# Optimization experiments

Hardware: AMD Instinct MI355X
Metric: run time of the kernel (lower is better)

Reference implementation:

```python
import jax, jax.numpy as jnp
import numpy as np

N, E = 50000, 800000
IN_DIM, HID, L, H = 128, 128, 3, 4
C = HID // H  # per-head channels
NEG_SLOPE = 0.2


def layer_norm(x, g, b, eps=1e-5):
    mu = jnp.mean(x, axis=-1, keepdims=True)
    var = jnp.var(x, axis=-1, keepdims=True)
    return (x - mu) * jax.lax.rsqrt(var + eps) * g + b


def gatv2_conv(x, edge_index, Wl, bl, Wr, br, att, conv_b):
    # x: [N, HID]; edge_index: [2, E]; Wl/Wr: [HID, HID]; att: [H, C]
    src, dst = edge_index[0], edge_index[1]
    xl = (x @ Wl + bl).reshape(N, H, C)  # source transform
    xr = (x @ Wr + br).reshape(N, H, C)  # target transform
    e = jax.nn.leaky_relu(xl[src] + xr[dst], NEG_SLOPE)      # [E, H, C]
    alpha = jnp.einsum('ehc,hc->eh', e, att)                  # [E, H]
    # segment softmax over incoming edges of each dst node
    amax = jax.ops.segment_max(alpha, dst, num_segments=N)    # [N, H]
    ex = jnp.exp(alpha - amax[dst])
    denom = jax.ops.segment_sum(ex, dst, num_segments=N)[dst] + 1e-16
    w = ex / denom                                            # [E, H]
    out = jax.ops.segment_sum(xl[src] * w[:, :, None], dst, num_segments=N)
    return out.reshape(N, HID) + conv_b


def setup_inputs() -> dict:
    key = jax.random.key(0)
    ks = jax.random.split(key, 24)
    s = 0.05
    inp = {
        'x': jax.random.normal(ks[0], (N, IN_DIM), jnp.float32),
        'edge_index': jax.random.randint(ks[1], (2, E), 0, N, jnp.int64),
        'Win': jax.random.normal(ks[2], (IN_DIM, HID)) * s,
        'b_in': jnp.zeros((HID,)),
        'ln_g': jnp.ones((L, HID)),
        'ln_b': jnp.zeros((L, HID)),
        'Wl': jax.random.normal(ks[3], (L, HID, HID)) * s,
        'bl': jnp.zeros((L, HID)),
        'Wr': jax.random.normal(ks[4], (L, HID, HID)) * s,
        'br': jnp.zeros((L, HID)),
        'att': jax.random.normal(ks[5], (L, H, C)) * s,
        'conv_b': jnp.zeros((L, HID)),
        'fn_g': jnp.ones((HID,)),
        'fn_b': jnp.zeros((HID,)),
        'pW1': jax.random.normal(ks[6], (HID, HID // 2)) * s,
        'pb1': jnp.zeros((HID // 2,)),
        'pW2': jax.random.normal(ks[7], (HID // 2, 1)) * s,
        'pb2': jnp.zeros((1,)),
        'vW1': jax.random.normal(ks[8], (HID, HID // 2)) * s,
        'vb1': jnp.zeros((HID // 2,)),
        'vW2': jax.random.normal(ks[9], (HID // 2, HID)) * s,
        'vb2': jnp.zeros((HID,)),
    }
    return inp


def reference(x, edge_index, Win, b_in, ln_g, ln_b, Wl, bl, Wr, br, att, conv_b,
              fn_g, fn_b, pW1, pb1, pW2, pb2, vW1, vb1, vW2, vb2):
    h = x @ Win + b_in  # input_proj
    # GNNResidualBlock (assumed pre-norm residual): h = h + gelu(conv(LN(h)))
    for i in range(L):
        z = layer_norm(h, ln_g[i], ln_b[i])
        z = gatv2_conv(z, edge_index, Wl[i], bl[i], Wr[i], br[i], att[i], conv_b[i])
        h = h + jax.nn.gelu(z)
    h = layer_norm(h, fn_g, fn_b)
    prob_logits = jax.nn.gelu(h @ pW1 + pb1) @ pW2 + pb2   # [N, 1]
    volume_emb = jax.nn.gelu(h @ vW1 + vb1) @ vW2 + vb2     # [N, HID]
    return (volume_emb, prob_logits)
```

## Files before the change

kernel.cpp:

```cpp
#include <hip/hip_runtime.h>
#include <math.h>

constexpr int NN  = 50000;
constexpr int EE  = 800000;
constexpr int NPAD = 50176;

typedef short bf16x8 __attribute__((ext_vector_type(8)));
typedef float f32x4  __attribute__((ext_vector_type(4)));

__device__ __forceinline__ unsigned f2bfu(float f) {
    union { float f; unsigned u; } x; x.f = f;
    unsigned r = x.u + 0x7fffu + ((x.u >> 16) & 1u);
    return r >> 16;
}
__device__ __forceinline__ short f2bf(float f) { return (short)f2bfu(f); }
__device__ __forceinline__ unsigned pack2(float lo, float hi) {
    return f2bfu(lo) | (f2bfu(hi) << 16);
}
__device__ __forceinline__ float bfbits_lo(unsigned w) { return __uint_as_float(w << 16); }
__device__ __forceinline__ float bfbits_hi(unsigned w) { return __uint_as_float(w & 0xffff0000u); }

__device__ __forceinline__ float gelu_tanh(float x) {
    float u = 0.7978845608028654f * (x + 0.044715f * x * x * x);
    float t = 1.0f - 2.0f / (__expf(2.0f * u) + 1.0f);
    return 0.5f * x * (1.0f + t);
}

__device__ __forceinline__ float dpp_add16(float x) {
    int t;
    t = __builtin_amdgcn_update_dpp(0, __float_as_int(x), 0xB1,  0xf, 0xf, true);
    x += __int_as_float(t);
    t = __builtin_amdgcn_update_dpp(0, __float_as_int(x), 0x4E,  0xf, 0xf, true);
    x += __int_as_float(t);
    t = __builtin_amdgcn_update_dpp(0, __float_as_int(x), 0x141, 0xf, 0xf, true);
    x += __int_as_float(t);
    t = __builtin_amdgcn_update_dpp(0, __float_as_int(x), 0x140, 0xf, 0xf, true);
    x += __int_as_float(t);
    return x;
}

struct WtArgs {
    const float* src[10];
    short*       dst[10];
    int K[10];
    int N[10];
};

template<int BN, int NB, int DO_LN, int ACT, int OUTBF0, int OUTBF1>
__device__ __forceinline__ void ln_gemm_body(
    int row0, const float* __restrict__ A,
    const float* __restrict__ lg, const float* __restrict__ lb,
    const short* __restrict__ B0t, const float* __restrict__ bias0, void* __restrict__ C0,
    const short* __restrict__ B1t, const float* __restrict__ bias1, void* __restrict__ C1,
    int nrows, short* As, short* Bs)
{
    constexpr int K = 128, KP = 136;
    constexpr int NF = BN / 16;
    constexpr int CH = K / 8;
    const int tid = threadIdx.x;

    {
        int r = tid >> 2, q = tid & 3;
        int grow = row0 + r;
        bool ok = grow < nrows;
        float4 v[8];
        const float* src = A + (size_t)grow * K + q * 32;
#pragma unroll
        for (int i = 0; i < 8; ++i)
            v[i] = ok ? *reinterpret_cast<const float4*>(src + i * 4)
                      : make_float4(0.f, 0.f, 0.f, 0.f);
        if (DO_LN) {
            float s = 0.f, s2 = 0.f;
#pragma unroll
            for (int i = 0; i < 8; ++i) {
                s  += v[i].x + v[i].y + v[i].z + v[i].w;
                s2 += v[i].x * v[i].x + v[i].y * v[i].y + v[i].z * v[i].z + v[i].w * v[i].w;
            }
            s += __shfl_xor(s, 1); s2 += __shfl_xor(s2, 1);
            s += __shfl_xor(s, 2); s2 += __shfl_xor(s2, 2);
            float mean = s * (1.f / 128.f);
            float var  = s2 * (1.f / 128.f) - mean * mean;
            float rstd = rsqrtf(var + 1e-5f);
#pragma unroll
            for (int i = 0; i < 8; ++i) {
                float4 gg = *reinterpret_cast<const float4*>(lg + q * 32 + i * 4);
                float4 bb = *reinterpret_cast<const float4*>(lb + q * 32 + i * 4);
                v[i].x = (v[i].x - mean) * rstd * gg.x + bb.x;
                v[i].y = (v[i].y - mean) * rstd * gg.y + bb.y;
                v[i].z = (v[i].z - mean) * rstd * gg.z + bb.z;
                v[i].w = (v[i].w - mean) * rstd * gg.w + bb.w;
            }
        }
        short* dst = &As[r * KP + q * 32];
#pragma unroll
        for (int i = 0; i < 4; ++i) {
            uint4 w = make_uint4(pack2(v[2*i].x,   v[2*i].y),
                                 pack2(v[2*i].z,   v[2*i].w),
                                 pack2(v[2*i+1].x, v[2*i+1].y),
                                 pack2(v[2*i+1].z, v[2*i+1].w));
            *reinterpret_cast<uint4*>(dst + i * 8) = w;
        }
    }

    auto stageB = [&](const short* __restrict__ Bt) {
#pragma unroll
        for (int it = 0; it < BN * CH / 256; ++it) {
            int idx = tid + it * 256;
            int nn = idx / CH, j = idx % CH;
            *reinterpret_cast<uint4*>(&Bs[nn * KP + j * 8]) =
                *reinterpret_cast<const uint4*>(&Bt[nn * K + j * 8]);
        }
    };
    stageB(B0t);
    __syncthreads();

    const int wave = tid >> 6;
    const int lane = tid & 63;
    const int kg   = lane >> 4;
    const int lr   = lane & 15;

    bf16x8 afrag[4];
#pragma unroll
    for (int kk = 0; kk < 4; ++kk)
        afrag[kk] = *reinterpret_cast<const bf16x8*>(
            &As[(wave * 16 + lr) * KP + kk * 32 + kg * 8]);

    auto do_gemm = [&](const float* __restrict__ bias, void* __restrict__ Cv, bool outbf) {
        f32x4 acc[NF];
#pragma unroll
        for (int nf = 0; nf < NF; ++nf) acc[nf] = (f32x4){0.f, 0.f, 0.f, 0.f};
#pragma unroll
        for (int nf = 0; nf < NF; ++nf) {
#pragma unroll
            for (int kk = 0; kk < 4; ++kk) {
                bf16x8 bfrag = *reinterpret_cast<const bf16x8*>(
                    &Bs[(nf * 16 + lr) * KP + kk * 32 + kg * 8]);
                acc[nf] = __builtin_amdgcn_mfma_f32_16x16x32_bf16(
                    afrag[kk], bfrag, acc[nf], 0, 0, 0);
            }
        }
#pragma unroll
        for (int nf = 0; nf < NF; ++nf) {
            int col = nf * 16 + lr;
            float bi = bias[col];
#pragma unroll
            for (int j = 0; j < 4; ++j) {
                int row = row0 + wave * 16 + kg * 4 + j;
                if (row < nrows) {
                    float v = acc[nf][j] + bi;
                    if (ACT == 1) v = gelu_tanh(v);
                    if (outbf) ((short*)Cv)[(size_t)row * BN + col] = f2bf(v);
                    else       ((float*)Cv)[(size_t)row * BN + col] = v;
                }
            }
        }
    };

    do_gemm(bias0, C0, OUTBF0 != 0);
    if (NB == 2) {
        __syncthreads();
        stageB(B1t);
        __syncthreads();
        do_gemm(bias1, C1, OUTBF1 != 0);
    }
}

__global__ __launch_bounds__(256) void hybrid1(
    const int* __restrict__ ei, int* __restrict__ counts, int* __restrict__ pos, WtArgs a)
{
    if (blockIdx.x < 1024) {
        for (int e = blockIdx.x * 256 + threadIdx.x; e < EE; e += 1024 * 256)
            pos[e] = atomicAdd(&counts[ei[EE + e]], 1);
    } else {
        int bb = blockIdx.x - 1024;
        int m = bb >> 4, slice = bb & 15;
        const float* s = a.src[m];
        short* d = a.dst[m];
        int K = a.K[m], N = a.N[m], total = K * N;
        for (int i = slice * 256 + threadIdx.x; i < total; i += 16 * 256) {
            int k = i / N, n = i - k * N;
            d[n * K + k] = f2bf(s[i]);
        }
    }
}

__device__ void scan256(const int* __restrict__ counts, int* __restrict__ roff) {
    __shared__ int wsum[4];
    __shared__ int tilesum;
    int tid = threadIdx.x, wid = tid >> 6, lane = tid & 63;
    int carry = 0;
    for (int base = 0; base < NPAD; base += 1024) {
        int idx = base + tid * 4;
        int4 c = *reinterpret_cast<const int4*>(&counts[idx]);
        int s0 = c.x, s1 = s0 + c.y, s2 = s1 + c.z, s3 = s2 + c.w;
        int x = s3;
#pragma unroll
        for (int off = 1; off < 64; off <<= 1) {
            int t = __shfl_up(x, off);
            if (lane >= off) x += t;
        }
        if (lane == 63) wsum[wid] = x;
        __syncthreads();
        if (tid == 0) {
            int a0 = wsum[0], a1 = wsum[1], a2 = wsum[2], a3 = wsum[3];
            wsum[0] = 0; wsum[1] = a0; wsum[2] = a0 + a1; wsum[3] = a0 + a1 + a2;
            tilesum = a0 + a1 + a2 + a3;
        }
        __syncthreads();
        int start = carry + wsum[wid] + (x - s3);
        int4 o = make_int4(start, start + s0, start + s1, start + s2);
        *reinterpret_cast<int4*>(&roff[idx]) = o;
        carry += tilesum;
        __syncthreads();
    }
}

__global__ __launch_bounds__(256) void hybrid2(
    const int* __restrict__ counts, int* __restrict__ roff,
    const float* __restrict__ x, const short* __restrict__ Win_t,
    const float* __restrict__ b_in, float* __restrict__ h, int nrows)
{
    __shared__ short As[64 * 136];
    __shared__ short Bs[128 * 136];
    if (blockIdx.x == 0) {
        scan256(counts, roff);
    } else {
        ln_gemm_body<128, 1, 0, 0, 0, 0>((blockIdx.x - 1) * 64, x, nullptr, nullptr,
            Win_t, b_in, h, nullptr, nullptr, nullptr, nrows, As, Bs);
    }
}

__global__ __launch_bounds__(256) void hybrid3(
    const int* __restrict__ ei, const int* __restrict__ roff,
    const int* __restrict__ pos, int* __restrict__ ssrc,
    const float* __restrict__ h, const float* __restrict__ lg, const float* __restrict__ lb,
    const short* __restrict__ Wl_t, const float* __restrict__ bl, short* __restrict__ XL,
    const short* __restrict__ Wr_t, const float* __restrict__ br, short* __restrict__ XR,
    int nrows)
{
    __shared__ short As[64 * 136];
    __shared__ short Bs[128 * 136];
    if (blockIdx.x < 512) {
        for (int e = blockIdx.x * 256 + threadIdx.x; e < EE; e += 512 * 256)
            ssrc[roff[ei[EE + e]] + pos[e]] = ei[e] << 8;
    } else {
        ln_gemm_body<128, 2, 1, 0, 1, 1>((blockIdx.x - 512) * 64, h, lg, lb,
            Wl_t, bl, XL, Wr_t, br, XR, nrows, As, Bs);
    }
}

__global__ __launch_bounds__(256) void fused_layer(
    const float* __restrict__ h, const float* __restrict__ lg, const float* __restrict__ lb,
    const short* __restrict__ Wl_t, const float* __restrict__ bl, short* __restrict__ XL,
    const short* __restrict__ Wr_t, const float* __restrict__ br, short* __restrict__ XR,
    int nrows)
{
    __shared__ short As[64 * 136];
    __shared__ short Bs[128 * 136];
    ln_gemm_body<128, 2, 1, 0, 1, 1>(blockIdx.x * 64, h, lg, lb,
        Wl_t, bl, XL, Wr_t, br, XR, nrows, As, Bs);
}

__global__ __launch_bounds__(256) void gat_node_kernel(
    const short* __restrict__ XL, const short* __restrict__ XR,
    const int* __restrict__ roff, const int* __restrict__ ssrc,
    const float* __restrict__ att, const float* __restrict__ conv_b,
    float* __restrict__ h)
{
    int n = blockIdx.x * 4 + (threadIdx.x >> 6);
    if (n >= NN) return;
    int lane = threadIdx.x & 63;
    int j0 = lane * 2;
    unsigned wr = *reinterpret_cast<const unsigned*>(&XR[(size_t)n * 128 + j0]);
    float xr0 = bfbits_lo(wr), xr1 = bfbits_hi(wr);
    float2 at = *reinterpret_cast<const float2*>(&att[j0]);

    float dA = 0.f, a0A = 0.f, a1A = 0.f;
    float dB = 0.f, a0B = 0.f, a1B = 0.f;

    const char* XLb = (const char*)XL;
    const unsigned lbyte = (unsigned)lane * 4u;

    auto proc = [&](unsigned w, float& d, float& a0, float& a1) {
        float x0 = bfbits_lo(w), x1 = bfbits_hi(w);
        float e0 = x0 + xr0; e0 = fmaxf(e0, 0.2f * e0);
        float e1 = x1 + xr1; e1 = fmaxf(e1, 0.2f * e1);
        float part = fmaf(e1, at.y, e0 * at.x);
        part = dpp_add16(part);
        float pe = __expf(part);
        d += pe;
        a0 = fmaf(pe, x0, a0);
        a1 = fmaf(pe, x1, a1);
    };

    int beg = roff[n], end = roff[n + 1], p = beg;
    for (; p + 3 < end; p += 4) {
        unsigned o0 = (unsigned)ssrc[p]     + lbyte;
        unsigned o1 = (unsigned)ssrc[p + 1] + lbyte;
        unsigned o2 = (unsigned)ssrc[p + 2] + lbyte;
        unsigned o3 = (unsigned)ssrc[p + 3] + lbyte;
        unsigned w0 = *reinterpret_cast<const unsigned*>(XLb + o0);
        unsigned w1 = *reinterpret_cast<const unsigned*>(XLb + o1);
        unsigned w2 = *reinterpret_cast<const unsigned*>(XLb + o2);
        unsigned w3 = *reinterpret_cast<const unsigned*>(XLb + o3);
        proc(w0, dA, a0A, a1A);
        proc(w1, dB, a0B, a1B);
        proc(w2, dA, a0A, a1A);
        proc(w3, dB, a0B, a1B);
    }
    for (; p < end; ++p) {
        unsigned w0 = *reinterpret_cast<const unsigned*>(
            XLb + ((unsigned)ssrc[p] + lbyte));
        proc(w0, dA, a0A, a1A);
    }
    float d    = dA + dB;
    float acc0 = a0A + a0B;
    float acc1 = a1A + a1B;

    float inv = 1.f / (d + 1e-16f);
    float2 cb = *reinterpret_cast<const float2*>(&conv_b[j0]);
    float o0 = gelu_tanh(fmaf(acc0, inv, cb.x));
    float o1 = gelu_tanh(fmaf(acc1, inv, cb.y));
    float2 hv = *reinterpret_cast<const float2*>(&h[(size_t)n * 128 + j0]);
    hv.x += o0; hv.y += o1;
    *reinterpret_cast<float2*>(&h[(size_t)n * 128 + j0]) = hv;
}

__global__ __launch_bounds__(256) void final_head_full(
    const float* __restrict__ A,
    const float* __restrict__ lg, const float* __restrict__ lb,
    const short* __restrict__ pW1t, const float* __restrict__ pb1,
    const float* __restrict__ pW2, const float* __restrict__ pb2,
    const short* __restrict__ vW1t, const float* __restrict__ vb1,
    const short* __restrict__ vW2t, const float* __restrict__ vb2,
    float* __restrict__ vol, float* __restrict__ prob, int nrows)
{
    constexpr int K = 128, KP = 136, KP2 = 72;
    constexpr int CH = K / 8;
    __shared__ short As[64 * 136];
    __shared__ short Bs[128 * 136];

    const int tid  = threadIdx.x;
    const int row0 = blockIdx.x * 64;

    {
        int r = tid >> 2, q = tid & 3;
        int grow = row0 + r;
        bool ok = grow < nrows;
        float4 v[8];
        const float* src = A + (size_t)grow * K + q * 32;
#pragma unroll
        for (int i = 0; i < 8; ++i)
            v[i] = ok ? *reinterpret_cast<const float4*>(src + i * 4)
                      : make_float4(0.f, 0.f, 0.f, 0.f);
        float s = 0.f, s2 = 0.f;
#pragma unroll
        for (int i = 0; i < 8; ++i) {
            s  += v[i].x + v[i].y + v[i].z + v[i].w;
            s2 += v[i].x * v[i].x + v[i].y * v[i].y + v[i].z * v[i].z + v[i].w * v[i].w;
        }
        s += __shfl_xor(s, 1); s2 += __shfl_xor(s2, 1);
        s += __shfl_xor(s, 2); s2 += __shfl_xor(s2, 2);
        float mean = s * (1.f / 128.f);
        float var  = s2 * (1.f / 128.f) - mean * mean;
        float rstd = rsqrtf(var + 1e-5f);
        short* dst = &As[r * KP + q * 32];
#pragma unroll
        for (int i = 0; i < 8; ++i) {
            float4 gg = *reinterpret_cast<const float4*>(lg + q * 32 + i * 4);
            float4 bb = *reinterpret_cast<const float4*>(lb + q * 32 + i * 4);
            v[i].x = (v[i].x - mean) * rstd * gg.x + bb.x;
            v[i].y = (v[i].y - mean) * rstd * gg.y + bb.y;
            v[i].z = (v[i].z - mean) * rstd * gg.z + bb.z;
            v[i].w = (v[i].w - mean) * rstd * gg.w + bb.w;
        }
#pragma unroll
        for (int i = 0; i < 4; ++i) {
            uint4 w = make_uint4(pack2(v[2*i].x,   v[2*i].y),
                                 pack2(v[2*i].z,   v[2*i].w),
                                 pack2(v[2*i+1].x, v[2*i+1].y),
                                 pack2(v[2*i+1].z, v[2*i+1].w));
            *reinterpret_cast<uint4*>(dst + i * 8) = w;
        }
    }
#pragma unroll
    for (int it = 0; it < 8; ++it) {
        int idx = tid + it * 256;
        int nn = idx / CH, j = idx % CH;
        const short* srcw = (nn < 64) ? &pW1t[nn * K + j * 8]
                                      : &vW1t[(nn - 64) * K + j * 8];
        *reinterpret_cast<uint4*>(&Bs[nn * KP + j * 8]) =
            *reinterpret_cast<const uint4*>(srcw);
    }
    __syncthreads();

    const int wave = tid >> 6;
    const int lane = tid & 63;
    const int kg   = lane >> 4;
    const int lr   = lane & 15;

    bf16x8 afrag[4];
#pragma unroll
    for (int kk = 0; kk < 4; ++kk)
        afrag[kk] = *reinterpret_cast<const bf16x8*>(
            &As[(wave * 16 + lr) * KP + kk * 32 + kg * 8]);

    f32x4 acc_v[4];
#pragma unroll
    for (int nf = 0; nf < 4; ++nf) acc_v[nf] = (f32x4){0.f, 0.f, 0.f, 0.f};
#pragma unroll
    for (int nf = 0; nf < 4; ++nf)
#pragma unroll
        for (int kk = 0; kk < 4; ++kk) {
            bf16x8 bfrag = *reinterpret_cast<const bf16x8*>(
                &Bs[(64 + nf * 16 + lr) * KP + kk * 32 + kg * 8]);
            acc_v[nf] = __builtin_amdgcn_mfma_f32_16x16x32_bf16(
                afrag[kk], bfrag, acc_v[nf], 0, 0, 0);
        }

    {
        f32x4 acc[4];
#pragma unroll
        for (int nf = 0; nf < 4; ++nf) acc[nf] = (f32x4){0.f, 0.f, 0.f, 0.f};
#pragma unroll
        for (int nf = 0; nf < 4; ++nf)
#pragma unroll
            for (int kk = 0; kk < 4; ++kk) {
                bf16x8 bfrag = *reinterpret_cast<const bf16x8*>(
                    &Bs[(nf * 16 + lr) * KP + kk * 32 + kg * 8]);
                acc[nf] = __builtin_amdgcn_mfma_f32_16x16x32_bf16(
                    afrag[kk], bfrag, acc[nf], 0, 0, 0);
            }
        float pr[4] = {0.f, 0.f, 0.f, 0.f};
#pragma unroll
        for (int nf = 0; nf < 4; ++nf) {
            int col = nf * 16 + lr;
            float bi = pb1[col];
            float w2 = pW2[col];
#pragma unroll
            for (int j = 0; j < 4; ++j)
                pr[j] = fmaf(gelu_tanh(acc[nf][j] + bi), w2, pr[j]);
        }
#pragma unroll
        for (int j = 0; j < 4; ++j) {
            float v = dpp_add16(pr[j]);
            int row = row0 + wave * 16 + kg * 4 + j;
            if (lr == 0 && row < nrows) prob[row] = v + pb2[0];
        }
    }

    __syncthreads();
    short* t2lds = As;
#pragma unroll
    for (int nf = 0; nf < 4; ++nf) {
        int col = nf * 16 + lr;
        float bi = vb1[col];
#pragma unroll
        for (int j = 0; j < 4; ++j) {
            int r = wave * 16 + kg * 4 + j;
            t2lds[r * KP2 + col] = f2bf(gelu_tanh(acc_v[nf][j] + bi));
        }
    }
#pragma unroll
    for (int it = 0; it < 4; ++it) {
        int idx = tid + it * 256;
        int nn = idx >> 3, j = idx & 7;
        *reinterpret_cast<uint4*>(&Bs[nn * KP2 + j * 8]) =
            *reinterpret_cast<const uint4*>(&vW2t[nn * 64 + j * 8]);
    }
    __syncthreads();

    bf16x8 a2[2];
#pragma unroll
    for (int kk = 0; kk < 2; ++kk)
        a2[kk] = *reinterpret_cast<const bf16x8*>(
            &t2lds[(wave * 16 + lr) * KP2 + kk * 32 + kg * 8]);
    f32x4 accv[8];
#pragma unroll
    for (int nf = 0; nf < 8; ++nf) accv[nf] = (f32x4){0.f, 0.f, 0.f, 0.f};
#pragma unroll
    for (int nf = 0; nf < 8; ++nf)
#pragma unroll
        for (int kk = 0; kk < 2; ++kk) {
            bf16x8 bfrag = *reinterpret_cast<const bf16x8*>(
                &Bs[(nf * 16 + lr) * KP2 + kk * 32 + kg * 8]);
            accv[nf] = __builtin_amdgcn_mfma_f32_16x16x32_bf16(
                a2[kk], bfrag, accv[nf], 0, 0, 0);
        }
#pragma unroll
    for (int nf = 0; nf < 8; ++nf) {
        int col = nf * 16 + lr;
        float bi = vb2[col];
#pragma unroll
        for (int j = 0; j < 4; ++j) {
            int row = row0 + wave * 16 + kg * 4 + j;
            if (row < nrows)
                vol[(size_t)row * 128 + col] = accv[nf][j] + bi;
        }
    }
}

extern "C" void kernel_launch(void* const* d_in, const int* in_sizes, int n_in,
                              void* d_out, int out_size, void* d_ws, size_t ws_size,
                              hipStream_t stream)
{
    const float* x      = (const float*)d_in[0];
    const int*   ei     = (const int*)  d_in[1];
    const float* Win    = (const float*)d_in[2];
    const float* b_in   = (const float*)d_in[3];
    const float* ln_g   = (const float*)d_in[4];
    const float* ln_b   = (const float*)d_in[5];
    const float* Wl     = (const float*)d_in[6];
    const float* bl     = (const float*)d_in[7];
    const float* Wr     = (const float*)d_in[8];
    const float* br     = (const float*)d_in[9];
    const float* att    = (const float*)d_in[10];
    const float* conv_b = (const float*)d_in[11];
    const float* fn_g   = (const float*)d_in[12];
    const float* fn_b   = (const float*)d_in[13];
    const float* pW1    = (const float*)d_in[14];
    const float* pb1    = (const float*)d_in[15];
    const float* pW2    = (const float*)d_in[16];
    const float* pb2    = (const float*)d_in[17];
    const float* vW1    = (const float*)d_in[18];
    const float* vb1    = (const float*)d_in[19];
    const float* vW2    = (const float*)d_in[20];
    const float* vb2    = (const float*)d_in[21];

    char* wp = (char*)d_ws;
    float* h   = (float*)wp;  wp += (size_t)NN * 128 * 4;
    short* XL  = (short*)wp;  wp += (size_t)NN * 128 * 2;
    short* XR  = (short*)wp;  wp += (size_t)NN * 128 * 2;
    int* counts = (int*)wp;   wp += (size_t)NPAD * 4;
    int* roff   = (int*)wp;   wp += (size_t)(NPAD + 16) * 4;
    int* pos    = (int*)wp;   wp += (size_t)EE * 4;
    int* ssrc   = (int*)wp;   wp += (size_t)EE * 4;
    short* Win_t = (short*)wp;
    short* Wl_t  = Win_t + 16384;
    short* Wr_t  = Wl_t + 3 * 16384;
    short* pW1_t = Wr_t + 3 * 16384;
    short* vW1_t = pW1_t + 8192;
    short* vW2_t = vW1_t + 8192;
    float* vol  = (float*)d_out;
    float* prob = (float*)d_out + (size_t)NN * 128;

    WtArgs wa;
    wa.src[0] = Win;  wa.dst[0] = Win_t; wa.K[0] = 128; wa.N[0] = 128;
    for (int i = 0; i < 3; ++i) {
        wa.src[1 + i] = Wl + (size_t)i * 16384; wa.dst[1 + i] = Wl_t + i * 16384;
        wa.K[1 + i] = 128; wa.N[1 + i] = 128;
        wa.src[4 + i] = Wr + (size_t)i * 16384; wa.dst[4 + i] = Wr_t + i * 16384;
        wa.K[4 + i] = 128; wa.N[4 + i] = 128;
    }
    wa.src[7] = pW1; wa.dst[7] = pW1_t; wa.K[7] = 128; wa.N[7] = 64;
    wa.src[8] = vW1; wa.dst[8] = vW1_t; wa.K[8] = 128; wa.N[8] = 64;
    wa.src[9] = vW2; wa.dst[9] = vW2_t; wa.K[9] = 64;  wa.N[9] = 128;

    const int gemm_grid = (NN + 63) / 64;
    const int row_grid  = (NN + 3) / 4;

    hipMemsetAsync(counts, 0, (size_t)NPAD * sizeof(int), stream);
    hybrid1<<<1024 + 160, 256, 0, stream>>>(ei, counts, pos, wa);
    hybrid2<<<1 + gemm_grid, 256, 0, stream>>>(counts, roff, x, Win_t, b_in, h, NN);
    hybrid3<<<512 + gemm_grid, 256, 0, stream>>>(ei, roff, pos, ssrc,
        h, ln_g, ln_b, Wl_t, bl, XL, Wr_t, br, XR, NN);
    gat_node_kernel<<<row_grid, 256, 0, stream>>>(
        XL, XR, roff, ssrc, att, conv_b, h);
    for (int i = 1; i < 3; ++i) {
        fused_layer<<<gemm_grid, 256, 0, stream>>>(
            h, ln_g + i * 128, ln_b + i * 128,
            Wl_t + i * 16384, bl + i * 128, XL,
            Wr_t + i * 16384, br + i * 128, XR, NN);
        gat_node_kernel<<<row_grid, 256, 0, stream>>>(
            XL, XR, roff, ssrc, att + i * 128, conv_b + i * 128, h);
    }
    final_head_full<<<gemm_grid, 256, 0, stream>>>(
        h, fn_g, fn_b, pW1_t, pb1, pW2, pb2, vW1_t, vb1, vW2_t, vb2, vol, prob, NN);
}
```

Measured before the change: 376.4 us.

## Replace stored edge positions with destination-partitioned atomic scatter; use exp2 in softmax

The CSR build no longer writes and reads back a per-edge position array. The scatter kernel now has each of 8 block groups handle one destination range and claim slots with a second atomic counter array, which removes 3.2MB of position traffic but makes every block scan its edge chunk 8 times. The attention softmax folds log2(e) into the attention vector and uses the native exp2 instruction instead of __expf. Edge order within each node becomes nondeterministic, which changes float summation order slightly.

```diff
diff --git a/kernel.cpp b/kernel.cpp
--- a/kernel.cpp
+++ b/kernel.cpp
@@ -4,6 +4,7 @@
 constexpr int NN  = 50000;
 constexpr int EE  = 800000;
 constexpr int NPAD = 50176;
+constexpr float LOG2E = 1.4426950408889634f;
 
 typedef short bf16x8 __attribute__((ext_vector_type(8)));
 typedef float f32x4  __attribute__((ext_vector_type(4)));
@@ -166,11 +167,11 @@
 }
 
 __global__ __launch_bounds__(256) void hybrid1(
-    const int* __restrict__ ei, int* __restrict__ counts, int* __restrict__ pos, WtArgs a)
+    const int* __restrict__ ei, int* __restrict__ counts, WtArgs a)
 {
     if (blockIdx.x < 1024) {
         for (int e = blockIdx.x * 256 + threadIdx.x; e < EE; e += 1024 * 256)
-            pos[e] = atomicAdd(&counts[ei[EE + e]], 1);
+            atomicAdd(&counts[ei[EE + e]], 1);
     } else {
         int bb = blockIdx.x - 1024;
         int m = bb >> 4, slice = bb & 15;
@@ -225,14 +226,14 @@
     if (blockIdx.x == 0) {
         scan256(counts, roff);
     } else {
-        ln_gemm_body<128, 1, 0, 0, 0, 0>((blockIdx.x - 1) * 64, x, nullptr, nullptr,
-            Win_t, b_in, h, nullptr, nullptr, nullptr, nrows, As, Bs);
+        ln_gemm_body<128, 1, 0, 0, 0, 0>((blockIdx.x - 1) * 64, x, nullptr,
+            nullptr, Win_t, b_in, h, nullptr, nullptr, nullptr, nrows, As, Bs);
     }
 }
 
 __global__ __launch_bounds__(256) void hybrid3(
     const int* __restrict__ ei, const int* __restrict__ roff,
-    const int* __restrict__ pos, int* __restrict__ ssrc,
+    int* __restrict__ cur, int* __restrict__ ssrc,
     const float* __restrict__ h, const float* __restrict__ lg, const float* __restrict__ lb,
     const short* __restrict__ Wl_t, const float* __restrict__ bl, short* __restrict__ XL,
     const short* __restrict__ Wr_t, const float* __restrict__ br, short* __restrict__ XR,
@@ -241,11 +242,19 @@
     __shared__ short As[64 * 136];
     __shared__ short Bs[128 * 136];
     if (blockIdx.x < 512) {
-        for (int e = blockIdx.x * 256 + threadIdx.x; e < EE; e += 512 * 256)
-            ssrc[roff[ei[EE + e]] + pos[e]] = ei[e] << 8;
+        int grp = blockIdx.x & 7, chunk = blockIdx.x >> 3;
+        int lo = grp * (NPAD / 8), hi = lo + (NPAD / 8);
+        int e0 = chunk * (EE / 64), e1 = e0 + (EE / 64);
+        for (int e = e0 + threadIdx.x; e < e1; e += 256) {
+            int d = ei[EE + e];
+            if (d >= lo && d < hi) {
+                int p = atomicAdd(&cur[d], 1);
+                ssrc[roff[d] + p] = ei[e] << 8;
+            }
+        }
     } else {
-        ln_gemm_body<128, 2, 1, 0, 1, 1>((blockIdx.x - 512) * 64, h, lg, lb,
-            Wl_t, bl, XL, Wr_t, br, XR, nrows, As, Bs);
+        ln_gemm_body<128, 2, 1, 0, 1, 1>((blockIdx.x - 512) * 64, h,
+            lg, lb, Wl_t, bl, XL, Wr_t, br, XR, nrows, As, Bs);
     }
 }
 
@@ -274,6 +283,7 @@
     unsigned wr = *reinterpret_cast<const unsigned*>(&XR[(size_t)n * 128 + j0]);
     float xr0 = bfbits_lo(wr), xr1 = bfbits_hi(wr);
     float2 at = *reinterpret_cast<const float2*>(&att[j0]);
+    float atx = at.x * LOG2E, aty = at.y * LOG2E;
 
     float dA = 0.f, a0A = 0.f, a1A = 0.f;
     float dB = 0.f, a0B = 0.f, a1B = 0.f;
@@ -285,9 +295,9 @@
         float x0 = bfbits_lo(w), x1 = bfbits_hi(w);
         float e0 = x0 + xr0; e0 = fmaxf(e0, 0.2f * e0);
         float e1 = x1 + xr1; e1 = fmaxf(e1, 0.2f * e1);
-        float part = fmaf(e1, at.y, e0 * at.x);
+        float part = fmaf(e1, aty, e0 * atx);
         part = dpp_add16(part);
-        float pe = __expf(part);
+        float pe = __builtin_amdgcn_exp2f(part);
         d += pe;
         a0 = fmaf(pe, x0, a0);
         a1 = fmaf(pe, x1, a1);
@@ -528,12 +538,12 @@
     const float* vb2    = (const float*)d_in[21];
 
     char* wp = (char*)d_ws;
-    float* h   = (float*)wp;  wp += (size_t)NN * 128 * 4;
-    short* XL  = (short*)wp;  wp += (size_t)NN * 128 * 2;
-    short* XR  = (short*)wp;  wp += (size_t)NN * 128 * 2;
+    float* h    = (float*)wp; wp += (size_t)NN * 128 * 4;
+    short* XL   = (short*)wp; wp += (size_t)NN * 128 * 2;
+    short* XR   = (short*)wp; wp += (size_t)NN * 128 * 2;
     int* counts = (int*)wp;   wp += (size_t)NPAD * 4;
+    int* cur    = (int*)wp;   wp += (size_t)NPAD * 4;
     int* roff   = (int*)wp;   wp += (size_t)(NPAD + 16) * 4;
-    int* pos    = (int*)wp;   wp += (size_t)EE * 4;
     int* ssrc   = (int*)wp;   wp += (size_t)EE * 4;
     short* Win_t = (short*)wp;
     short* Wl_t  = Win_t + 16384;
@@ -541,6 +551,7 @@
     short* pW1_t = Wr_t + 3 * 16384;
     short* vW1_t = pW1_t + 8192;
     short* vW2_t = vW1_t + 8192;
+    short* t2 = XL;
     float* vol  = (float*)d_out;
     float* prob = (float*)d_out + (size_t)NN * 128;
 
@@ -559,10 +570,10 @@
     const int gemm_grid = (NN + 63) / 64;
     const int row_grid  = (NN + 3) / 4;
 
-    hipMemsetAsync(counts, 0, (size_t)NPAD * sizeof(int), stream);
-    hybrid1<<<1024 + 160, 256, 0, stream>>>(ei, counts, pos, wa);
+    hipMemsetAsync(counts, 0, (size_t)2 * NPAD * sizeof(int), stream);
+    hybrid1<<<1024 + 160, 256, 0, stream>>>(ei, counts, wa);
     hybrid2<<<1 + gemm_grid, 256, 0, stream>>>(counts, roff, x, Win_t, b_in, h, NN);
-    hybrid3<<<512 + gemm_grid, 256, 0, stream>>>(ei, roff, pos, ssrc,
+    hybrid3<<<512 + gemm_grid, 256, 0, stream>>>(ei, roff, cur, ssrc,
         h, ln_g, ln_b, Wl_t, bl, XL, Wr_t, br, XR, NN);
     gat_node_kernel<<<row_grid, 256, 0, stream>>>(
         XL, XR, roff, ssrc, att, conv_b, h);
```

After: 404.2 us. +7.4%, slower.
